# Optimization experiments

Measured on AMD Instinct MI355X. Metric: run time of the kernel, lower is better.

## Reference

```python
import jax, jax.numpy as jnp
import numpy as np

N_HEADS = 16
MASK_FILL = -2.0**15 + 1.0  # -32767, matches torch reference


def setup_inputs() -> dict:
    key = jax.random.key(0)
    ks = jax.random.split(key, 10)
    B, N, D = 4, 2048, 1024
    sc = 0.02
    return {
        "q": jax.random.normal(ks[0], (B, N, D), jnp.float32),
        "k": jax.random.normal(ks[1], (B, N, D), jnp.float32),
        "v": jax.random.normal(ks[2], (B, N, D), jnp.float32),
        "Wq": jax.random.normal(ks[3], (D, D), jnp.float32) * sc,
        "bq": jnp.zeros((D,), jnp.float32),
        "Wk": jax.random.normal(ks[4], (D, D), jnp.float32) * sc,
        "bk": jnp.zeros((D,), jnp.float32),
        "Wv": jax.random.normal(ks[5], (D, D), jnp.float32) * sc,
        "bv": jnp.zeros((D,), jnp.float32),
        "Wo": jax.random.normal(ks[6], (D, D), jnp.float32) * sc,
    }


def reference(q, k, v, Wq, bq, Wk, bk, Wv, bv, Wo):
    B, N, D = q.shape
    H = N_HEADS
    dh = D // H
    scale = dh ** (-0.5)

    def proj(x, W, b):
        # torch nn.Linear: x @ W.T + b, W stored as (out, in)
        y = jnp.einsum('bnd,od->bno', x, W) + b
        return y.reshape(B, N, H, dh).transpose(0, 2, 1, 3)  # b h n d

    qh = proj(q, Wq, bq)
    kh = proj(k, Wk, bk)
    vh = proj(v, Wv, bv)

    scores = jnp.einsum('bhnd,bhmd->bhnm', qh, kh) * scale  # [B,H,N,N]
    causal = jnp.tril(jnp.ones((N, N), dtype=bool))
    scores = jnp.where(causal, scores, jnp.float32(MASK_FILL))
    attn = jax.nn.softmax(scores, axis=-1)
    x = jnp.einsum('bhnm,bhmd->bhnd', attn, vh)
    x = x.transpose(0, 2, 1, 3).reshape(B, N, D)  # b n (h d)
    return jnp.einsum('bnd,od->bno', x, Wo)  # to_out Linear, bias=False; dropout p=0
```

## Files before the change

### kernel.cpp

```cpp
#include <hip/hip_runtime.h>
#include <hip/hip_bf16.h>
#include <cstdint>
#include <cstddef>

typedef __bf16 bf16_t;
typedef __bf16 bf16x4 __attribute__((ext_vector_type(4)));
typedef __bf16 bf16x8 __attribute__((ext_vector_type(8)));
typedef float  f32x4  __attribute__((ext_vector_type(4)));

static constexpr int Bsz  = 4;
static constexpr int Nseq = 2048;
static constexpr int Dmod = 1024;
static constexpr int H    = 16;
static constexpr int DH   = 64;
static constexpr int M_TOT = Bsz * Nseq;
static constexpr int K    = 1024;
static constexpr int BM = 128, BN = 128, BK = 32;

__device__ __forceinline__ f32x4 mfma16(bf16x8 a, bf16x8 b, f32x4 c) {
  return __builtin_amdgcn_mfma_f32_16x16x32_bf16(a, b, c, 0, 0, 0);
}

__device__ __forceinline__ bf16x8 cvt8(const float* p) {
  f32x4 lo = *(const f32x4*)(p);
  f32x4 hi = *(const f32x4*)(p + 4);
  bf16x8 r;
#pragma unroll
  for (int i = 0; i < 4; ++i) { r[i] = (bf16_t)lo[i]; r[4 + i] = (bf16_t)hi[i]; }
  return r;
}

__device__ __forceinline__ void async16(const bf16_t* g, bf16_t* l) {
  __builtin_amdgcn_global_load_lds(
      (const __attribute__((address_space(1))) void*)g,
      (__attribute__((address_space(3))) void*)l, 16, 0, 0);
}

struct CvtArgs {
  const float* src[7];
  bf16_t* dst[7];
  int n[7];
};

__global__ __launch_bounds__(256) void cvt_kernel(CvtArgs a) {
  const int z = blockIdx.y;
  const float* s = a.src[z];
  bf16x8* d = (bf16x8*)a.dst[z];
  const int n8 = a.n[z] >> 3;
  const int stride = gridDim.x * 256;
  for (int i = blockIdx.x * 256 + threadIdx.x; i < n8; i += stride)
    d[i] = cvt8(s + (size_t)i * 8);
}

template <int MODE, typename CT>
__device__ __forceinline__ void gemm_body(
    bf16_t (*As)[BK], bf16_t (*Ws)[BK],
    const bf16_t* __restrict__ A, const bf16_t* __restrict__ W,
    const float* __restrict__ bias, CT* __restrict__ C, float oscale) {
  const int tid  = threadIdx.x;
  const int lane = tid & 63;
  const int wave = tid >> 6;
  const int wm = wave & 1, wn = wave >> 1;
  const int row = lane & 15, quad = lane >> 4;

  const int m_blk = blockIdx.x * BM;
  const int n_blk = blockIdx.y * BN;

  f32x4 acc[4][4];
#pragma unroll
  for (int i = 0; i < 4; ++i)
#pragma unroll
    for (int j = 0; j < 4; ++j) acc[i][j] = (f32x4){0.f, 0.f, 0.f, 0.f};

  const int srow = lane >> 2;
  const int scol = (lane & 3) * 8;

  const bf16_t* Abase = A + (size_t)m_blk * K + scol;
  const bf16_t* Wbase = W + (size_t)n_blk * K + scol;

  for (int k0 = 0; k0 < K; k0 += BK) {
#pragma unroll
    for (int j = 0; j < 2; ++j) {
      const int seg = wave * 2 + j;
      async16(Abase + (size_t)(seg * 16 + srow) * K + k0, &As[seg * 16][0]);
      async16(Wbase + (size_t)(seg * 16 + srow) * K + k0, &Ws[seg * 16][0]);
    }
    __syncthreads();

    bf16x8 af[4], wf[4];
#pragma unroll
    for (int i = 0; i < 4; ++i)
      af[i] = *(const bf16x8*)(&As[wm * 64 + i * 16 + row][quad * 8]);
#pragma unroll
    for (int i = 0; i < 4; ++i)
      wf[i] = *(const bf16x8*)(&Ws[wn * 64 + i * 16 + row][quad * 8]);
#pragma unroll
    for (int i = 0; i < 4; ++i)
#pragma unroll
      for (int j = 0; j < 4; ++j) {
        if (MODE == 1)
          acc[i][j] = mfma16(af[i], wf[j], acc[i][j]);
        else
          acc[i][j] = mfma16(wf[j], af[i], acc[i][j]);
      }
    __syncthreads();
  }

  if (MODE == 0) {
#pragma unroll
    for (int i = 0; i < 4; ++i) {
      const int m = m_blk + wm * 64 + i * 16 + row;
      const int b = m >> 11, n = m & 2047;
#pragma unroll
      for (int j = 0; j < 4; ++j) {
        const int o0 = n_blk + wn * 64 + j * 16 + quad * 4;
        const int hh = o0 >> 6, od = o0 & 63;
        const f32x4 bv4 = *(const f32x4*)(bias + o0);
        const size_t idx0 = (((size_t)b * H + hh) * Nseq + n) * DH + od;
        bf16x4 pkt;
#pragma unroll
        for (int r = 0; r < 4; ++r)
          pkt[r] = (bf16_t)((acc[i][j][r] + bv4[r]) * oscale);
        *(bf16x4*)((bf16_t*)C + idx0) = pkt;
      }
    }
  } else if (MODE == 2) {
#pragma unroll
    for (int i = 0; i < 4; ++i) {
      const int m = m_blk + wm * 64 + i * 16 + row;
#pragma unroll
      for (int j = 0; j < 4; ++j) {
        const int o0 = n_blk + wn * 64 + j * 16 + quad * 4;
        *(f32x4*)((float*)C + (size_t)m * Dmod + o0) = acc[i][j];
      }
    }
  } else {
#pragma unroll
    for (int j = 0; j < 4; ++j) {
      const int o = n_blk + wn * 64 + j * 16 + row;
      const float bv = bias[o];
      const int hh = o >> 6, od = o & 63;
#pragma unroll
      for (int i = 0; i < 4; ++i) {
        const int m0 = m_blk + wm * 64 + i * 16 + quad * 4;
        const int b = m0 >> 11, n = m0 & 2047;
        const size_t idx0 = (((size_t)b * H + hh) * DH + od) * Nseq + n;
        bf16x4 pkt;
#pragma unroll
        for (int r = 0; r < 4; ++r)
          pkt[r] = (bf16_t)(acc[i][j][r] + bv);
        *(bf16x4*)((bf16_t*)C + idx0) = pkt;
      }
    }
  }
}

struct QkvArgs {
  const bf16_t* A[3];
  const bf16_t* W[3];
  const float*  bias[3];
  bf16_t*       out[3];
};

__global__ __launch_bounds__(256) void qkv_gemm(QkvArgs a, float qscale) {
  __shared__ bf16_t As[BM][BK];
  __shared__ bf16_t Ws[BN][BK];
  const int z = blockIdx.z;
  if (z == 2)
    gemm_body<1, bf16_t>(As, Ws, a.A[2], a.W[2], a.bias[2], a.out[2], 1.f);
  else if (z == 1)
    gemm_body<0, bf16_t>(As, Ws, a.A[1], a.W[1], a.bias[1], a.out[1], 1.f);
  else
    gemm_body<0, bf16_t>(As, Ws, a.A[0], a.W[0], a.bias[0], a.out[0], qscale);
}

__global__ __launch_bounds__(256) void out_gemm(
    const bf16_t* __restrict__ A, const bf16_t* __restrict__ W,
    float* __restrict__ C) {
  __shared__ bf16_t As[BM][BK];
  __shared__ bf16_t Ws[BN][BK];
  gemm_body<2, float>(As, Ws, A, W, nullptr, C, 1.f);
}

__global__ __launch_bounds__(256, 4) void attn_fwd(
    const bf16_t* __restrict__ Q, const bf16_t* __restrict__ Kh,
    const bf16_t* __restrict__ VT, bf16_t* __restrict__ X) {
  const int lane = threadIdx.x & 63;
  const int wave = threadIdx.x >> 6;
  const int bid = blockIdx.x;
  const int bh = (bid & 7) * 8 + ((bid >> 3) & 7);
  const int qt = 31 - (bid >> 6);
  const int b = bh >> 4, h = bh & 15;
  const int row = lane & 15, quad = lane >> 4;

  __shared__ __align__(16) bf16_t Kt[2][32][64];
  __shared__ __align__(16) bf16_t Vt[2][64][32];
  __shared__ __align__(16) bf16_t plds[4][16][56];

  const bf16_t* Qb = Q + (size_t)bh * Nseq * DH;
  const bf16_t* Kb = Kh + (size_t)bh * Nseq * DH;
  const bf16_t* Vb = VT + (size_t)bh * DH * Nseq;

  const int krow_l = lane >> 3;
  const int kc8    = lane & 7;
  const bf16_t* ksrc =
      Kb + (size_t)(wave * 8 + krow_l) * DH + (kc8 ^ krow_l) * 8;
  bf16_t* kdst = &Kt[0][wave * 8][0];

  const int vd_l = lane >> 2;
  const int vkc  = lane & 3;
  const int vd   = wave * 16 + vd_l;
  const bf16_t* vsrc =
      Vb + (size_t)vd * Nseq + (vkc ^ ((vd_l >> 1) & 3)) * 8;
  bf16_t* vdst = &Vt[0][wave * 16][0];

  auto stage = [&](int t, int buf) {
    async16(ksrc + (size_t)t * (32 * DH), kdst + buf * (32 * 64));
    async16(vsrc + t * 32, vdst + buf * (64 * 32));
  };

  const int q0 = qt * 64 + wave * 16;
  const int qg = q0 + row;

  bf16x8 qf0 = *(const bf16x8*)(Qb + (size_t)(q0 + row) * DH + quad * 8);
  bf16x8 qf1 = *(const bf16x8*)(Qb + (size_t)(q0 + row) * DH + 32 + quad * 8);

  f32x4 o_acc[4];
#pragma unroll
  for (int c = 0; c < 4; ++c) o_acc[c] = (f32x4){0.f, 0.f, 0.f, 0.f};
  f32x4 ls2[2];
  ls2[0] = (f32x4){0.f, 0.f, 0.f, 0.f};
  ls2[1] = (f32x4){0.f, 0.f, 0.f, 0.f};

  auto tile_body = [&](int it, int buf, bool mask) {
    bf16x8 kf[2][2], vf[4];
#pragma unroll
    for (int c = 0; c < 2; ++c)
#pragma unroll
      for (int hf = 0; hf < 2; ++hf)
        kf[c][hf] = *(const bf16x8*)(
            &Kt[buf][c * 16 + row][((hf * 4 + quad) ^ (row & 7)) * 8]);
#pragma unroll
    for (int ch = 0; ch < 4; ++ch)
      vf[ch] = *(const bf16x8*)(
          &Vt[buf][ch * 16 + row][(quad ^ ((row >> 1) & 3)) * 8]);

    f32x4 s[2];
    __builtin_amdgcn_s_setprio(1);
#pragma unroll
    for (int c = 0; c < 2; ++c) {
      s[c] = (f32x4){0.f, 0.f, 0.f, 0.f};
      s[c] = mfma16(kf[c][0], qf0, s[c]);
      s[c] = mfma16(kf[c][1], qf1, s[c]);
    }
    __builtin_amdgcn_s_setprio(0);

    const int k0 = it * 32;
#pragma unroll
    for (int c = 0; c < 2; ++c) {
      bf16x4 pk;
      f32x4 pv4;
#pragma unroll
      for (int r = 0; r < 4; ++r) {
        float t = s[c][r];
        if (mask) {
          const int kg = k0 + c * 16 + quad * 4 + r;
          t = (kg <= qg) ? t : -1e38f;
        }
        float pv = __builtin_amdgcn_exp2f(t);
        pv4[r] = pv;
        pk[r] = (bf16_t)pv;
      }
      ls2[c] += pv4;
      *(bf16x4*)(&plds[wave][row][c * 16 + quad * 4]) = pk;
    }
    __asm__ volatile("s_waitcnt lgkmcnt(0)" ::: "memory");
    const bf16x8 pf = *(const bf16x8*)(&plds[wave][row][quad * 8]);
    __builtin_amdgcn_s_setprio(1);
#pragma unroll
    for (int ch = 0; ch < 4; ++ch)
      o_acc[ch] = mfma16(pf, vf[ch], o_acc[ch]);
    __builtin_amdgcn_s_setprio(0);
  };

  const int nfull = 2 * qt;

  stage(0, 0);

#pragma unroll 1
  for (int it = 0; it < nfull; ++it) {
    const int buf = it & 1;
    __syncthreads();
    stage(it + 1, buf ^ 1);
    tile_body(it, buf, false);
  }
#pragma unroll 1
  for (int e = 0; e < 2; ++e) {
    const int it = nfull + e;
    const int buf = it & 1;
    __syncthreads();
    if (e == 0) stage(it + 1, buf ^ 1);
    tile_body(it, buf, true);
  }

  float ls = (ls2[0][0] + ls2[0][1]) + (ls2[0][2] + ls2[0][3]) +
             (ls2[1][0] + ls2[1][1]) + (ls2[1][2] + ls2[1][3]);
  ls += __shfl_xor(ls, 16, 64);
  ls += __shfl_xor(ls, 32, 64);

#pragma unroll
  for (int r = 0; r < 4; ++r) {
    const float linv = 1.f / __shfl(ls, quad * 4 + r, 64);
    const int qq = q0 + quad * 4 + r;
    const size_t base = ((size_t)b * Nseq + qq) * Dmod + h * DH;
#pragma unroll
    for (int ch = 0; ch < 4; ++ch)
      X[base + ch * 16 + row] = (bf16_t)(o_acc[ch][r] * linv);
  }
}

extern "C" void kernel_launch(void* const* d_in, const int* in_sizes, int n_in,
                              void* d_out, int out_size, void* d_ws,
                              size_t ws_size, hipStream_t stream) {
  const float* q  = (const float*)d_in[0];
  const float* k  = (const float*)d_in[1];
  const float* v  = (const float*)d_in[2];
  const float* Wq = (const float*)d_in[3];
  const float* bq = (const float*)d_in[4];
  const float* Wk = (const float*)d_in[5];
  const float* bk = (const float*)d_in[6];
  const float* Wv = (const float*)d_in[7];
  const float* bv = (const float*)d_in[8];
  const float* Wo = (const float*)d_in[9];
  float* out = (float*)d_out;

  const size_t E  = (size_t)M_TOT * Dmod;
  const size_t EW = (size_t)Dmod * Dmod;
  bf16_t* ws = (bf16_t*)d_ws;
  bf16_t* qb  = ws;
  bf16_t* kb  = ws + E;
  bf16_t* vb  = ws + 2 * E;
  bf16_t* Wqb = ws + 3 * E;
  bf16_t* Wkb = Wqb + EW;
  bf16_t* Wvb = Wkb + EW;
  bf16_t* Wob = Wvb + EW;
  bf16_t* Qh  = Wob + EW;
  bf16_t* Kh  = Qh + E;
  bf16_t* VT  = Kh + E;
  bf16_t* X   = kb;

  CvtArgs ca;
  ca.src[0] = q;  ca.dst[0] = qb;  ca.n[0] = (int)E;
  ca.src[1] = k;  ca.dst[1] = kb;  ca.n[1] = (int)E;
  ca.src[2] = v;  ca.dst[2] = vb;  ca.n[2] = (int)E;
  ca.src[3] = Wq; ca.dst[3] = Wqb; ca.n[3] = (int)EW;
  ca.src[4] = Wk; ca.dst[4] = Wkb; ca.n[4] = (int)EW;
  ca.src[5] = Wv; ca.dst[5] = Wvb; ca.n[5] = (int)EW;
  ca.src[6] = Wo; ca.dst[6] = Wob; ca.n[6] = (int)EW;
  cvt_kernel<<<dim3(512, 7), 256, 0, stream>>>(ca);

  const float C_SC = 0.125f * 1.44269504088896f;

  dim3 blk(256);
  QkvArgs qa;
  qa.A[0] = qb; qa.W[0] = Wqb; qa.bias[0] = bq; qa.out[0] = Qh;
  qa.A[1] = kb; qa.W[1] = Wkb; qa.bias[1] = bk; qa.out[1] = Kh;
  qa.A[2] = vb; qa.W[2] = Wvb; qa.bias[2] = bv; qa.out[2] = VT;
  qkv_gemm<<<dim3(M_TOT / BM, Dmod / BN, 3), blk, 0, stream>>>(qa, C_SC);

  attn_fwd<<<dim3(2048), blk, 0, stream>>>(Qh, Kh, VT, X);

  out_gemm<<<dim3(M_TOT / BM, Dmod / BN), blk, 0, stream>>>(X, Wob, out);
}
```

Baseline: 320.7 us.

## Triple-buffer LDS staging with vmcnt waits in GEMMs and attention

Converts the GEMM k-loop and the attention K/V loop from single or double buffering to a three-stage LDS ring. Two tiles are prefetched ahead, and each iteration waits on vmcnt and uses a single s_barrier instead of two __syncthreads. The goal is to hide global-load latency and remove one barrier per iteration. In exchange LDS use grows, which may lower occupancy. Correctness now depends on the hand-counted vmcnt values matching the async loads each wave issues.

```diff
diff --git a/kernel.cpp b/kernel.cpp
--- a/kernel.cpp
+++ b/kernel.cpp
@@ -17,6 +17,8 @@
 static constexpr int K    = 1024;
 static constexpr int BM = 128, BN = 128, BK = 32;
 
+#define WAITVM(N) asm volatile("s_waitcnt vmcnt(" #N ")" ::: "memory")
+
 __device__ __forceinline__ f32x4 mfma16(bf16x8 a, bf16x8 b, f32x4 c) {
   return __builtin_amdgcn_mfma_f32_16x16x32_bf16(a, b, c, 0, 0, 0);
 }
@@ -54,7 +56,7 @@
 
 template <int MODE, typename CT>
 __device__ __forceinline__ void gemm_body(
-    bf16_t (*As)[BK], bf16_t (*Ws)[BK],
+    bf16_t (*As)[BM][BK], bf16_t (*Ws)[BN][BK],
     const bf16_t* __restrict__ A, const bf16_t* __restrict__ W,
     const float* __restrict__ bias, CT* __restrict__ C, float oscale) {
   const int tid  = threadIdx.x;
@@ -78,22 +80,38 @@
   const bf16_t* Abase = A + (size_t)m_blk * K + scol;
   const bf16_t* Wbase = W + (size_t)n_blk * K + scol;
 
-  for (int k0 = 0; k0 < K; k0 += BK) {
+  constexpr int NT = K / BK;
+
+  auto stage = [&](int t, int buf) {
 #pragma unroll
     for (int j = 0; j < 2; ++j) {
       const int seg = wave * 2 + j;
-      async16(Abase + (size_t)(seg * 16 + srow) * K + k0, &As[seg * 16][0]);
-      async16(Wbase + (size_t)(seg * 16 + srow) * K + k0, &Ws[seg * 16][0]);
-    }
-    __syncthreads();
+      async16(Abase + (size_t)(seg * 16 + srow) * K + t * BK,
+              &As[buf][seg * 16][0]);
+      async16(Wbase + (size_t)(seg * 16 + srow) * K + t * BK,
+              &Ws[buf][seg * 16][0]);
+    }
+  };
+
+  stage(0, 0);
+  stage(1, 1);
+  int buf = 0, bufn = 2;
+
+#pragma unroll 1
+  for (int it = 0; it < NT; ++it) {
+    if (it + 1 < NT) { WAITVM(4); } else { WAITVM(0); }
+    __builtin_amdgcn_s_barrier();
 
     bf16x8 af[4], wf[4];
 #pragma unroll
     for (int i = 0; i < 4; ++i)
-      af[i] = *(const bf16x8*)(&As[wm * 64 + i * 16 + row][quad * 8]);
+      af[i] = *(const bf16x8*)(&As[buf][wm * 64 + i * 16 + row][quad * 8]);
 #pragma unroll
     for (int i = 0; i < 4; ++i)
-      wf[i] = *(const bf16x8*)(&Ws[wn * 64 + i * 16 + row][quad * 8]);
+      wf[i] = *(const bf16x8*)(&Ws[buf][wn * 64 + i * 16 + row][quad * 8]);
+
+    if (it + 2 < NT) stage(it + 2, bufn);
+
 #pragma unroll
     for (int i = 0; i < 4; ++i)
 #pragma unroll
@@ -103,7 +121,9 @@
         else
           acc[i][j] = mfma16(wf[j], af[i], acc[i][j]);
       }
-    __syncthreads();
+
+    buf  = (buf  == 2) ? 0 : buf  + 1;
+    bufn = (bufn == 2) ? 0 : bufn + 1;
   }
 
   if (MODE == 0) {
@@ -163,8 +183,8 @@
 };
 
 __global__ __launch_bounds__(256) void qkv_gemm(QkvArgs a, float qscale) {
-  __shared__ bf16_t As[BM][BK];
-  __shared__ bf16_t Ws[BN][BK];
+  __shared__ bf16_t As[3][BM][BK];
+  __shared__ bf16_t Ws[3][BN][BK];
   const int z = blockIdx.z;
   if (z == 2)
     gemm_body<1, bf16_t>(As, Ws, a.A[2], a.W[2], a.bias[2], a.out[2], 1.f);
@@ -177,8 +197,8 @@
 __global__ __launch_bounds__(256) void out_gemm(
     const bf16_t* __restrict__ A, const bf16_t* __restrict__ W,
     float* __restrict__ C) {
-  __shared__ bf16_t As[BM][BK];
-  __shared__ bf16_t Ws[BN][BK];
+  __shared__ bf16_t As[3][BM][BK];
+  __shared__ bf16_t Ws[3][BN][BK];
   gemm_body<2, float>(As, Ws, A, W, nullptr, C, 1.f);
 }
 
@@ -193,8 +213,8 @@
   const int b = bh >> 4, h = bh & 15;
   const int row = lane & 15, quad = lane >> 4;
 
-  __shared__ __align__(16) bf16_t Kt[2][32][64];
-  __shared__ __align__(16) bf16_t Vt[2][64][32];
+  __shared__ __align__(16) bf16_t Kt[3][32][64];
+  __shared__ __align__(16) bf16_t Vt[3][64][32];
   __shared__ __align__(16) bf16_t plds[4][16][56];
 
   const bf16_t* Qb = Q + (size_t)bh * Nseq * DH;
@@ -232,7 +252,18 @@
   ls2[0] = (f32x4){0.f, 0.f, 0.f, 0.f};
   ls2[1] = (f32x4){0.f, 0.f, 0.f, 0.f};
 
-  auto tile_body = [&](int it, int buf, bool mask) {
+  const int nfull = 2 * qt;
+  const int NT = nfull + 2;
+
+  stage(0, 0);
+  stage(1, 1);
+  int buf = 0, bufn = 2;
+
+#pragma unroll 1
+  for (int it = 0; it < NT; ++it) {
+    if (it + 1 < NT) { WAITVM(2); } else { WAITVM(0); }
+    __builtin_amdgcn_s_barrier();
+
     bf16x8 kf[2][2], vf[4];
 #pragma unroll
     for (int c = 0; c < 2; ++c)
@@ -244,6 +275,8 @@
     for (int ch = 0; ch < 4; ++ch)
       vf[ch] = *(const bf16x8*)(
           &Vt[buf][ch * 16 + row][(quad ^ ((row >> 1) & 3)) * 8]);
+
+    if (it + 2 < NT) stage(it + 2, bufn);
 
     f32x4 s[2];
     __builtin_amdgcn_s_setprio(1);
@@ -255,6 +288,7 @@
     }
     __builtin_amdgcn_s_setprio(0);
 
+    const bool mask = (it >= nfull);
     const int k0 = it * 32;
 #pragma unroll
     for (int c = 0; c < 2; ++c) {
@@ -281,26 +315,9 @@
     for (int ch = 0; ch < 4; ++ch)
       o_acc[ch] = mfma16(pf, vf[ch], o_acc[ch]);
     __builtin_amdgcn_s_setprio(0);
-  };
-
-  const int nfull = 2 * qt;
-
-  stage(0, 0);
-
-#pragma unroll 1
-  for (int it = 0; it < nfull; ++it) {
-    const int buf = it & 1;
-    __syncthreads();
-    stage(it + 1, buf ^ 1);
-    tile_body(it, buf, false);
-  }
-#pragma unroll 1
-  for (int e = 0; e < 2; ++e) {
-    const int it = nfull + e;
-    const int buf = it & 1;
-    __syncthreads();
-    if (e == 0) stage(it + 1, buf ^ 1);
-    tile_body(it, buf, true);
+
+    buf  = (buf  == 2) ? 0 : buf  + 1;
+    bufn = (bufn == 2) ? 0 : bufn + 1;
   }
 
   float ls = (ls2[0][0] + ls2[0][1]) + (ls2[0][2] + ls2[0][3]) +
```

Result: no change. 317.1 us (-1.1%).
